# Kernel tuning notes

Measured on AMD Instinct MI355X. Metric: run time of the kernel, lower is better.

## Reference

```python
import jax, jax.numpy as jnp
import numpy as np

N_NODES = 50000
N_EDGES = 640000
IN_CH = 128
OUT_CH = 128


def setup_inputs() -> dict:
    key = jax.random.key(0)
    k1, k2, k3, k4 = jax.random.split(key, 4)
    x = jax.random.normal(k1, (N_NODES, IN_CH), dtype=jnp.float32)
    edge_index = jax.random.randint(k2, (2, N_EDGES), 0, N_NODES, dtype=jnp.int32)
    # nn.Linear params: W [out, in], b [out]
    bound = 1.0 / np.sqrt(IN_CH)
    W = jax.random.uniform(k3, (OUT_CH, IN_CH), minval=-bound, maxval=bound, dtype=jnp.float32)
    b = jax.random.uniform(k4, (OUT_CH,), minval=-bound, maxval=bound, dtype=jnp.float32)
    return {"x": x, "edge_index": edge_index, "W": W, "b": b}


def reference(x, edge_index, W, b):
    row, col = edge_index[0], edge_index[1]
    num_nodes = x.shape[0]
    # degree of each destination node (clamped to >= 1)
    deg = jax.ops.segment_sum(jnp.ones(row.shape[0], dtype=x.dtype), row,
                              num_segments=num_nodes)
    deg = jnp.maximum(deg, 1.0)
    # gather neighbor features and scatter-add into destinations
    agg = jax.ops.segment_sum(x[col], row, num_segments=num_nodes)
    agg = agg / deg[:, None]
    # residual + linear
    return (x + agg) @ W.T + b
```

## Files before the change

kernel.cpp:

```cpp
#include <hip/hip_runtime.h>

#define N_NODES 50000
#define N_EDGES 640000
#define CH 128
#define NBINS 1563
#define NTILES 1563
#define FILLB 64
#define EPB 10000
#define OBW (NBINS + 1)
#define CAPR 48

typedef __bf16 bf16_t;
typedef bf16_t bf16x8 __attribute__((ext_vector_type(8)));
typedef float f32x4 __attribute__((ext_vector_type(4)));

__device__ __forceinline__ ushort f2bf(float f) {
  union { float f; unsigned u; } v; v.f = f;
  unsigned r = v.u + 0x7FFFu + ((v.u >> 16) & 1u);
  return (ushort)(r >> 16);
}
__device__ __forceinline__ float bflo(unsigned u) {
  union { unsigned u; float f; } v; v.u = u << 16; return v.f;
}
__device__ __forceinline__ float bfhi(unsigned u) {
  union { unsigned u; float f; } v; v.u = u & 0xFFFF0000u; return v.f;
}
__device__ __forceinline__ unsigned pack2(float lo, float hi) {
  return (unsigned)f2bf(lo) | ((unsigned)f2bf(hi) << 16);
}
__device__ __forceinline__ void addrow(float* acc, uint4 v) {
  acc[0] += bflo(v.x); acc[1] += bfhi(v.x);
  acc[2] += bflo(v.y); acc[3] += bfhi(v.y);
  acc[4] += bflo(v.z); acc[5] += bfhi(v.z);
  acc[6] += bflo(v.w); acc[7] += bfhi(v.w);
}


__global__ __launch_bounds__(256) void fill_conv(const int* __restrict__ row,
                                                 const int* __restrict__ col,
                                                 unsigned* __restrict__ binRec,
                                                 ushort* __restrict__ obo,
                                                 const float4* __restrict__ x4,
                                                 uint4* __restrict__ xb4,
                                                 const float4* __restrict__ W4,
                                                 uint4* __restrict__ Wb4) {
  __shared__ int cnt[NBINS];
  __shared__ int parts[256];
  __shared__ __align__(16) unsigned recbuf[EPB];
  int bid = blockIdx.x;
  int tid = threadIdx.x;
  if (bid < FILLB) {
    for (int i = tid; i < NBINS; i += 256) cnt[i] = 0;
    __syncthreads();
    int base = bid * EPB;
    unsigned pk[40];
#pragma unroll
    for (int k = 0; k < 40; ++k) {
      int idx = tid + k * 256;
      pk[k] = 0xFFFFFFFFu;
      if (idx < EPB) {
        int rr = row[base + idx];
        int bi = rr >> 5;
        int rk = atomicAdd(&cnt[bi], 1);
        pk[k] = ((unsigned)bi << 8) | (unsigned)rk;
      }
    }
    __syncthreads();
    int c7[7];
    int s = 0;
#pragma unroll
    for (int k = 0; k < 7; ++k) {
      int i = tid * 7 + k;
      int c = (i < NBINS) ? cnt[i] : 0;
      c7[k] = c; s += c;
    }
    parts[tid] = s;
    __syncthreads();
    for (int off = 1; off < 256; off <<= 1) {
      int v = (tid >= off) ? parts[tid - off] : 0;
      __syncthreads();
      parts[tid] += v;
      __syncthreads();
    }
    int run = (tid > 0) ? parts[tid - 1] : 0;
    ushort* orow = obo + bid * OBW;
#pragma unroll
    for (int k = 0; k < 7; ++k) {
      int i = tid * 7 + k;
      if (i < NBINS) {
        orow[i] = (ushort)run;
        cnt[i] = run;
        run += c7[k];
      }
    }
    if (tid == 0) orow[NBINS] = (ushort)EPB;
    __syncthreads();
#pragma unroll
    for (int k = 0; k < 40; ++k) {
      int idx = tid + k * 256;
      if (idx < EPB) {
        unsigned p = pk[k];
        int bi = (int)(p >> 8);
        int rk = (int)(p & 255u);
        int rr = row[base + idx];
        int cc = col[base + idx];
        recbuf[cnt[bi] + rk] = ((unsigned)(rr & 31) << 16) | (unsigned)cc;
      }
    }
    __syncthreads();
    uint4* gb4 = (uint4*)(binRec + base);
    const uint4* rb4 = (const uint4*)recbuf;
    for (int j = tid; j < EPB / 4; j += 256) gb4[j] = rb4[j];
  } else if (bid < FILLB + 3125) {
    int i = (bid - FILLB) * 256 + tid;
    float4 a = x4[i * 2], b = x4[i * 2 + 1];
    uint4 o;
    o.x = pack2(a.x, a.y); o.y = pack2(a.z, a.w);
    o.z = pack2(b.x, b.y); o.w = pack2(b.z, b.w);
    xb4[i] = o;
  } else {
    for (int i = tid; i < 2048; i += 256) {
      float4 c = W4[i * 2], d = W4[i * 2 + 1];
      uint4 w;
      w.x = pack2(c.x, c.y); w.y = pack2(c.z, c.w);
      w.z = pack2(d.x, d.y); w.w = pack2(d.z, d.w);
      Wb4[i] = w;
    }
  }
}

__global__ __launch_bounds__(512) void fused(const uint4* __restrict__ xb4,
                                             const unsigned* __restrict__ binRec,
                                             const ushort* __restrict__ obo,
                                             const uint4* __restrict__ Wb4,
                                             const float4* __restrict__ bias4,
                                             float4* __restrict__ out4) {
  __shared__ ushort hT[32 * CH];
  __shared__ __align__(16) ushort colL[32 * CAPR];
  __shared__ int rowcnt[32];
  int tid = threadIdx.x;
  int g = blockIdx.x;
  int m0 = g * 32;

  if (tid < 32) rowcnt[tid] = 0;
  __syncthreads();
  if (tid < 256) {
    int i = tid >> 2, sub = tid & 3;
    const ushort* orow = obo + i * OBW + g;
    int o0 = orow[0], o1 = orow[1];
    const unsigned* rbase = binRec + i * EPB;
    for (int p = o0 + sub; p < o1; p += 4) {
      unsigned rec = rbase[p];
      int lr = (int)(rec >> 16);
      int pp = atomicAdd(&rowcnt[lr], 1);
      if (pp < CAPR) colL[lr * CAPR + pp] = (ushort)(rec & 0xFFFFu);
    }
  }
  __syncthreads();

  int wv = tid >> 6;
  int lane = tid & 63;
  int q = lane & 15;
  int grp = lane >> 4;
  int r = wv * 4 + grp;
  int node = m0 + r;
  int deg = rowcnt[r];
  int degc = deg < CAPR ? deg : CAPR;
  const ushort* arow = colL + r * CAPR;
  int nc = node < N_NODES ? node : 0;
  uint4 xi = xb4[nc * 16 + q];
  float acc[8] = {0.f, 0.f, 0.f, 0.f, 0.f, 0.f, 0.f, 0.f};
  int e = 0;
  for (; e + 7 < degc; e += 8) {
    uint4 ids = *(const uint4*)(arow + e);
    int n0 = ids.x & 0xFFFF, n1 = ids.x >> 16;
    int n2 = ids.y & 0xFFFF, n3 = ids.y >> 16;
    int n4 = ids.z & 0xFFFF, n5 = ids.z >> 16;
    int n6 = ids.w & 0xFFFF, n7 = ids.w >> 16;
    uint4 v0 = xb4[n0 * 16 + q];
    uint4 v1 = xb4[n1 * 16 + q];
    uint4 v2 = xb4[n2 * 16 + q];
    uint4 v3 = xb4[n3 * 16 + q];
    uint4 v4 = xb4[n4 * 16 + q];
    uint4 v5 = xb4[n5 * 16 + q];
    uint4 v6 = xb4[n6 * 16 + q];
    uint4 v7 = xb4[n7 * 16 + q];
    addrow(acc, v0); addrow(acc, v1); addrow(acc, v2); addrow(acc, v3);
    addrow(acc, v4); addrow(acc, v5); addrow(acc, v6); addrow(acc, v7);
  }
  if (e + 3 < degc) {
    uint2 ids = *(const uint2*)(arow + e);
    int n0 = ids.x & 0xFFFF, n1 = ids.x >> 16;
    int n2 = ids.y & 0xFFFF, n3 = ids.y >> 16;
    uint4 v0 = xb4[n0 * 16 + q];
    uint4 v1 = xb4[n1 * 16 + q];
    uint4 v2 = xb4[n2 * 16 + q];
    uint4 v3 = xb4[n3 * 16 + q];
    addrow(acc, v0); addrow(acc, v1); addrow(acc, v2); addrow(acc, v3);
    e += 4;
  }
  for (; e < degc; ++e) {
    uint4 v = xb4[(int)arow[e] * 16 + q];
    addrow(acc, v);
  }
  uint4 o = make_uint4(0, 0, 0, 0);
  if (node < N_NODES) {
    float s = 1.0f / fmaxf((float)deg, 1.0f);
    o.x = pack2(bflo(xi.x) + acc[0] * s, bfhi(xi.x) + acc[1] * s);
    o.y = pack2(bflo(xi.y) + acc[2] * s, bfhi(xi.y) + acc[3] * s);
    o.z = pack2(bflo(xi.z) + acc[4] * s, bfhi(xi.z) + acc[5] * s);
    o.w = pack2(bflo(xi.w) + acc[6] * s, bfhi(xi.w) + acc[7] * s);
  }
  *(uint4*)&hT[r * CH + ((q ^ (r & 15)) << 3)] = o;
  __syncthreads();

  int qq = grp;
  int mt = wv & 1;
  int nbase = (wv >> 1) * 2;
  const ushort* hbase = &hT[(mt * 16 + q) * CH];
  bf16x8 hb0 = *(const bf16x8*)(hbase + (((qq + 0) ^ q) << 3));
  bf16x8 hb1 = *(const bf16x8*)(hbase + (((qq + 4) ^ q) << 3));
  bf16x8 hb2 = *(const bf16x8*)(hbase + (((qq + 8) ^ q) << 3));
  bf16x8 hb3 = *(const bf16x8*)(hbase + (((qq + 12) ^ q) << 3));
  int m = m0 + mt * 16 + q;
#pragma unroll
  for (int i = 0; i < 2; ++i) {
    int nt = nbase + i;
    const uint4* wr = Wb4 + (nt * 16 + q) * 16 + qq;
    bf16x8 w0 = __builtin_bit_cast(bf16x8, wr[0]);
    bf16x8 w1 = __builtin_bit_cast(bf16x8, wr[4]);
    bf16x8 w2 = __builtin_bit_cast(bf16x8, wr[8]);
    bf16x8 w3 = __builtin_bit_cast(bf16x8, wr[12]);
    f32x4 acc2 = {0.f, 0.f, 0.f, 0.f};
    acc2 = __builtin_amdgcn_mfma_f32_16x16x32_bf16(w0, hb0, acc2, 0, 0, 0);
    acc2 = __builtin_amdgcn_mfma_f32_16x16x32_bf16(w1, hb1, acc2, 0, 0, 0);
    acc2 = __builtin_amdgcn_mfma_f32_16x16x32_bf16(w2, hb2, acc2, 0, 0, 0);
    acc2 = __builtin_amdgcn_mfma_f32_16x16x32_bf16(w3, hb3, acc2, 0, 0, 0);
    if (m < N_NODES) {
      float4 bv = bias4[nt * 4 + qq];
      f32x4 ov;
      ov.x = acc2[0] + bv.x;
      ov.y = acc2[1] + bv.y;
      ov.z = acc2[2] + bv.z;
      ov.w = acc2[3] + bv.w;
      __builtin_nontemporal_store(ov, (f32x4*)(out4 + (size_t)m * 32 + nt * 4 + qq));
    }
  }
}

extern "C" void kernel_launch(void* const* d_in, const int* in_sizes, int n_in,
                              void* d_out, int out_size, void* d_ws, size_t ws_size,
                              hipStream_t stream) {
  const float* x  = (const float*)d_in[0];
  const int*   ei = (const int*)d_in[1];
  const float* W  = (const float*)d_in[2];
  const float* bb = (const float*)d_in[3];

  char* ws = (char*)d_ws;
  unsigned* binRec = (unsigned*)ws;
  ushort*   obo    = (ushort*)(ws + 2560000);
  uint4*    Wb4    = (uint4*)(ws + 2760192);
  uint4*    xb4    = (uint4*)(ws + 2792960);

  fill_conv<<<FILLB + 3125 + 1, 256, 0, stream>>>(ei, ei + N_EDGES, binRec, obo,
                                                  (const float4*)x, xb4,
                                                  (const float4*)W, Wb4);
  fused<<<NTILES, 512, 0, stream>>>(xb4, binRec, obo, Wb4,
                                    (const float4*)bb, (float4*)d_out);
}
```

Before: 133.7 us.

## Double fill blocks, vectorize edge loads, halve fused block size

```diff
diff --git a/kernel.cpp b/kernel.cpp
--- a/kernel.cpp
+++ b/kernel.cpp
@@ -5,8 +5,8 @@
 #define CH 128
 #define NBINS 1563
 #define NTILES 1563
-#define FILLB 64
-#define EPB 10000
+#define FILLB 128
+#define EPB 5000
 #define OBW (NBINS + 1)
 #define CAPR 48
 
@@ -53,16 +53,37 @@
     for (int i = tid; i < NBINS; i += 256) cnt[i] = 0;
     __syncthreads();
     int base = bid * EPB;
-    unsigned pk[40];
-#pragma unroll
-    for (int k = 0; k < 40; ++k) {
-      int idx = tid + k * 256;
-      pk[k] = 0xFFFFFFFFu;
-      if (idx < EPB) {
-        int rr = row[base + idx];
-        int bi = rr >> 5;
-        int rk = atomicAdd(&cnt[bi], 1);
-        pk[k] = ((unsigned)bi << 8) | (unsigned)rk;
+    int4 r4s[5], c4s[5];
+    bool val[5];
+#pragma unroll
+    for (int b = 0; b < 5; ++b) {
+      int idx4 = b * 1024 + tid * 4;
+      val[b] = idx4 < EPB;
+      if (val[b]) {
+        r4s[b] = *(const int4*)(row + base + idx4);
+        c4s[b] = *(const int4*)(col + base + idx4);
+      }
+    }
+    unsigned pkv[20];
+    unsigned colp[10];
+#pragma unroll
+    for (int b = 0; b < 5; ++b) {
+      if (val[b]) {
+        int rr[4] = {r4s[b].x, r4s[b].y, r4s[b].z, r4s[b].w};
+        int cc[4] = {c4s[b].x, c4s[b].y, c4s[b].z, c4s[b].w};
+#pragma unroll
+        for (int j = 0; j < 4; ++j) {
+          int bi = rr[j] >> 5;
+          int rk = atomicAdd(&cnt[bi], 1);
+          pkv[b * 4 + j] = ((unsigned)bi << 13) |
+                           ((unsigned)(rr[j] & 31) << 8) | (unsigned)rk;
+        }
+        colp[b * 2]     = ((unsigned)cc[0] & 0xFFFFu) | ((unsigned)cc[1] << 16);
+        colp[b * 2 + 1] = ((unsigned)cc[2] & 0xFFFFu) | ((unsigned)cc[3] << 16);
+      } else {
+#pragma unroll
+        for (int j = 0; j < 4; ++j) pkv[b * 4 + j] = 0xFFFFFFFFu;
+        colp[b * 2] = 0; colp[b * 2 + 1] = 0;
       }
     }
     __syncthreads();
@@ -96,15 +117,14 @@
     if (tid == 0) orow[NBINS] = (ushort)EPB;
     __syncthreads();
 #pragma unroll
-    for (int k = 0; k < 40; ++k) {
-      int idx = tid + k * 256;
-      if (idx < EPB) {
-        unsigned p = pk[k];
-        int bi = (int)(p >> 8);
+    for (int k = 0; k < 20; ++k) {
+      unsigned p = pkv[k];
+      if (p != 0xFFFFFFFFu) {
+        int bi = (int)(p >> 13);
+        int lr5 = (int)((p >> 8) & 31u);
         int rk = (int)(p & 255u);
-        int rr = row[base + idx];
-        int cc = col[base + idx];
-        recbuf[cnt[bi] + rk] = ((unsigned)(rr & 31) << 16) | (unsigned)cc;
+        unsigned cw = (colp[k >> 1] >> ((k & 1) * 16)) & 0xFFFFu;
+        recbuf[cnt[bi] + rk] = ((unsigned)lr5 << 16) | cw;
       }
     }
     __syncthreads();
@@ -129,7 +149,7 @@
   }
 }
 
-__global__ __launch_bounds__(512) void fused(const uint4* __restrict__ xb4,
+__global__ __launch_bounds__(256) void fused(const uint4* __restrict__ xb4,
                                              const unsigned* __restrict__ binRec,
                                              const ushort* __restrict__ obo,
                                              const uint4* __restrict__ Wb4,
@@ -144,13 +164,13 @@
 
   if (tid < 32) rowcnt[tid] = 0;
   __syncthreads();
-  if (tid < 256) {
-    int i = tid >> 2, sub = tid & 3;
+  {
+    int i = tid >> 1, sub = tid & 1;
     const ushort* orow = obo + i * OBW + g;
     int o0 = orow[0], o1 = orow[1];
     const unsigned* rbase = binRec + i * EPB;
-    for (int p = o0 + sub; p < o1; p += 4) {
-      unsigned rec = rbase[p];
+    for (int p = o0 + sub; p < o1; p += 2) {
+      unsigned rec = __builtin_nontemporal_load(rbase + p);
       int lr = (int)(rec >> 16);
       int pp = atomicAdd(&rowcnt[lr], 1);
       if (pp < CAPR) colL[lr * CAPR + pp] = (ushort)(rec & 0xFFFFu);
@@ -162,61 +182,64 @@
   int lane = tid & 63;
   int q = lane & 15;
   int grp = lane >> 4;
-  int r = wv * 4 + grp;
-  int node = m0 + r;
-  int deg = rowcnt[r];
-  int degc = deg < CAPR ? deg : CAPR;
-  const ushort* arow = colL + r * CAPR;
-  int nc = node < N_NODES ? node : 0;
-  uint4 xi = xb4[nc * 16 + q];
-  float acc[8] = {0.f, 0.f, 0.f, 0.f, 0.f, 0.f, 0.f, 0.f};
-  int e = 0;
-  for (; e + 7 < degc; e += 8) {
-    uint4 ids = *(const uint4*)(arow + e);
-    int n0 = ids.x & 0xFFFF, n1 = ids.x >> 16;
-    int n2 = ids.y & 0xFFFF, n3 = ids.y >> 16;
-    int n4 = ids.z & 0xFFFF, n5 = ids.z >> 16;
-    int n6 = ids.w & 0xFFFF, n7 = ids.w >> 16;
-    uint4 v0 = xb4[n0 * 16 + q];
-    uint4 v1 = xb4[n1 * 16 + q];
-    uint4 v2 = xb4[n2 * 16 + q];
-    uint4 v3 = xb4[n3 * 16 + q];
-    uint4 v4 = xb4[n4 * 16 + q];
-    uint4 v5 = xb4[n5 * 16 + q];
-    uint4 v6 = xb4[n6 * 16 + q];
-    uint4 v7 = xb4[n7 * 16 + q];
-    addrow(acc, v0); addrow(acc, v1); addrow(acc, v2); addrow(acc, v3);
-    addrow(acc, v4); addrow(acc, v5); addrow(acc, v6); addrow(acc, v7);
-  }
-  if (e + 3 < degc) {
-    uint2 ids = *(const uint2*)(arow + e);
-    int n0 = ids.x & 0xFFFF, n1 = ids.x >> 16;
-    int n2 = ids.y & 0xFFFF, n3 = ids.y >> 16;
-    uint4 v0 = xb4[n0 * 16 + q];
-    uint4 v1 = xb4[n1 * 16 + q];
-    uint4 v2 = xb4[n2 * 16 + q];
-    uint4 v3 = xb4[n3 * 16 + q];
-    addrow(acc, v0); addrow(acc, v1); addrow(acc, v2); addrow(acc, v3);
-    e += 4;
-  }
-  for (; e < degc; ++e) {
-    uint4 v = xb4[(int)arow[e] * 16 + q];
-    addrow(acc, v);
-  }
-  uint4 o = make_uint4(0, 0, 0, 0);
-  if (node < N_NODES) {
-    float s = 1.0f / fmaxf((float)deg, 1.0f);
-    o.x = pack2(bflo(xi.x) + acc[0] * s, bfhi(xi.x) + acc[1] * s);
-    o.y = pack2(bflo(xi.y) + acc[2] * s, bfhi(xi.y) + acc[3] * s);
-    o.z = pack2(bflo(xi.z) + acc[4] * s, bfhi(xi.z) + acc[5] * s);
-    o.w = pack2(bflo(xi.w) + acc[6] * s, bfhi(xi.w) + acc[7] * s);
-  }
-  *(uint4*)&hT[r * CH + ((q ^ (r & 15)) << 3)] = o;
+#pragma unroll
+  for (int t = 0; t < 2; ++t) {
+    int r = wv * 8 + t * 4 + grp;
+    int node = m0 + r;
+    int deg = rowcnt[r];
+    int degc = deg < CAPR ? deg : CAPR;
+    const ushort* arow = colL + r * CAPR;
+    int nc = node < N_NODES ? node : 0;
+    uint4 xi = xb4[nc * 16 + q];
+    float acc[8] = {0.f, 0.f, 0.f, 0.f, 0.f, 0.f, 0.f, 0.f};
+    int e = 0;
+    for (; e + 7 < degc; e += 8) {
+      uint4 ids = *(const uint4*)(arow + e);
+      int n0 = ids.x & 0xFFFF, n1 = ids.x >> 16;
+      int n2 = ids.y & 0xFFFF, n3 = ids.y >> 16;
+      int n4 = ids.z & 0xFFFF, n5 = ids.z >> 16;
+      int n6 = ids.w & 0xFFFF, n7 = ids.w >> 16;
+      uint4 v0 = xb4[n0 * 16 + q];
+      uint4 v1 = xb4[n1 * 16 + q];
+      uint4 v2 = xb4[n2 * 16 + q];
+      uint4 v3 = xb4[n3 * 16 + q];
+      uint4 v4 = xb4[n4 * 16 + q];
+      uint4 v5 = xb4[n5 * 16 + q];
+      uint4 v6 = xb4[n6 * 16 + q];
+      uint4 v7 = xb4[n7 * 16 + q];
+      addrow(acc, v0); addrow(acc, v1); addrow(acc, v2); addrow(acc, v3);
+      addrow(acc, v4); addrow(acc, v5); addrow(acc, v6); addrow(acc, v7);
+    }
+    if (e + 3 < degc) {
+      uint2 ids = *(const uint2*)(arow + e);
+      int n0 = ids.x & 0xFFFF, n1 = ids.x >> 16;
+      int n2 = ids.y & 0xFFFF, n3 = ids.y >> 16;
+      uint4 v0 = xb4[n0 * 16 + q];
+      uint4 v1 = xb4[n1 * 16 + q];
+      uint4 v2 = xb4[n2 * 16 + q];
+      uint4 v3 = xb4[n3 * 16 + q];
+      addrow(acc, v0); addrow(acc, v1); addrow(acc, v2); addrow(acc, v3);
+      e += 4;
+    }
+    for (; e < degc; ++e) {
+      uint4 v = xb4[(int)arow[e] * 16 + q];
+      addrow(acc, v);
+    }
+    uint4 o = make_uint4(0, 0, 0, 0);
+    if (node < N_NODES) {
+      float s = 1.0f / fmaxf((float)deg, 1.0f);
+      o.x = pack2(bflo(xi.x) + acc[0] * s, bfhi(xi.x) + acc[1] * s);
+      o.y = pack2(bflo(xi.y) + acc[2] * s, bfhi(xi.y) + acc[3] * s);
+      o.z = pack2(bflo(xi.z) + acc[4] * s, bfhi(xi.z) + acc[5] * s);
+      o.w = pack2(bflo(xi.w) + acc[6] * s, bfhi(xi.w) + acc[7] * s);
+    }
+    *(uint4*)&hT[r * CH + ((q ^ (r & 15)) << 3)] = o;
+  }
   __syncthreads();
 
   int qq = grp;
   int mt = wv & 1;
-  int nbase = (wv >> 1) * 2;
+  int nbase = (wv >> 1) * 4;
   const ushort* hbase = &hT[(mt * 16 + q) * CH];
   bf16x8 hb0 = *(const bf16x8*)(hbase + (((qq + 0) ^ q) << 3));
   bf16x8 hb1 = *(const bf16x8*)(hbase + (((qq + 4) ^ q) << 3));
@@ -224,26 +247,26 @@
   bf16x8 hb3 = *(const bf16x8*)(hbase + (((qq + 12) ^ q) << 3));
   int m = m0 + mt * 16 + q;
 #pragma unroll
-  for (int i = 0; i < 2; ++i) {
+  for (int i = 0; i < 4; ++i) {
     int nt = nbase + i;
     const uint4* wr = Wb4 + (nt * 16 + q) * 16 + qq;
     bf16x8 w0 = __builtin_bit_cast(bf16x8, wr[0]);
     bf16x8 w1 = __builtin_bit_cast(bf16x8, wr[4]);
     bf16x8 w2 = __builtin_bit_cast(bf16x8, wr[8]);
     bf16x8 w3 = __builtin_bit_cast(bf16x8, wr[12]);
-    f32x4 acc2 = {0.f, 0.f, 0.f, 0.f};
-    acc2 = __builtin_amdgcn_mfma_f32_16x16x32_bf16(w0, hb0, acc2, 0, 0, 0);
-    acc2 = __builtin_amdgcn_mfma_f32_16x16x32_bf16(w1, hb1, acc2, 0, 0, 0);
-    acc2 = __builtin_amdgcn_mfma_f32_16x16x32_bf16(w2, hb2, acc2, 0, 0, 0);
-    acc2 = __builtin_amdgcn_mfma_f32_16x16x32_bf16(w3, hb3, acc2, 0, 0, 0);
+    f32x4 acc = {0.f, 0.f, 0.f, 0.f};
+    acc = __builtin_amdgcn_mfma_f32_16x16x32_bf16(w0, hb0, acc, 0, 0, 0);
+    acc = __builtin_amdgcn_mfma_f32_16x16x32_bf16(w1, hb1, acc, 0, 0, 0);
+    acc = __builtin_amdgcn_mfma_f32_16x16x32_bf16(w2, hb2, acc, 0, 0, 0);
+    acc = __builtin_amdgcn_mfma_f32_16x16x32_bf16(w3, hb3, acc, 0, 0, 0);
     if (m < N_NODES) {
       float4 bv = bias4[nt * 4 + qq];
-      f32x4 ov;
-      ov.x = acc2[0] + bv.x;
-      ov.y = acc2[1] + bv.y;
-      ov.z = acc2[2] + bv.z;
-      ov.w = acc2[3] + bv.w;
-      __builtin_nontemporal_store(ov, (f32x4*)(out4 + (size_t)m * 32 + nt * 4 + qq));
+      f32x4 o;
+      o.x = acc[0] + bv.x;
+      o.y = acc[1] + bv.y;
+      o.z = acc[2] + bv.z;
+      o.w = acc[3] + bv.w;
+      __builtin_nontemporal_store(o, (f32x4*)(out4 + (size_t)m * 32 + nt * 4 + qq));
     }
   }
 }
@@ -259,12 +282,12 @@
   char* ws = (char*)d_ws;
   unsigned* binRec = (unsigned*)ws;
   ushort*   obo    = (ushort*)(ws + 2560000);
-  uint4*    Wb4    = (uint4*)(ws + 2760192);
-  uint4*    xb4    = (uint4*)(ws + 2792960);
+  uint4*    Wb4    = (uint4*)(ws + 2960384);
+  uint4*    xb4    = (uint4*)(ws + 2993152);
 
   fill_conv<<<FILLB + 3125 + 1, 256, 0, stream>>>(ei, ei + N_EDGES, binRec, obo,
                                                   (const float4*)x, xb4,
                                                   (const float4*)W, Wb4);
-  fused<<<NTILES, 512, 0, stream>>>(xb4, binRec, obo, Wb4,
+  fused<<<NTILES, 256, 0, stream>>>(xb4, binRec, obo, Wb4,
                                     (const float4*)bb, (float4*)d_out);
 }
```

Result: no change. 131.8 us (-1.4%).
